# Performance work log

Measured on AMD Instinct MI355X. Metric: run time of the kernel, lower is better.

The kernel has to match this reference:

```python
import jax, jax.numpy as jnp
import numpy as np

# ---- config (matches init_kwargs) ----
SPATIAL_SCALE = 0.0625
POOLED = 7
OUT_DIM = 256
SAMPLE_PER_PART = 4
TRANS_STD = 0.1
PART_SIZE = 7
DEFORM_FC_DIM = 1024
# group_size == 1 -> position-sensitive group index is always 0, channel c == ctop


def _deform_roi_pool(feat, rois, offset, no_trans):
    """Faithful JAX port of DeformablePSROIPoolForward (DCNv2), group_size=1.
    feat: (B,C,H,W), rois: (N,5)=[b,x1,y1,x2,y2], offset: (N,2,P,P) or None.
    Returns (N,C,P,P)."""
    B, C, H, W = feat.shape
    N = rois.shape[0]
    P, S = POOLED, SAMPLE_PER_PART
    dt = feat.dtype
    featT = jnp.transpose(feat, (0, 2, 3, 1))  # (B,H,W,C) for spatial gathers

    b = rois[:, 0].astype(jnp.int32)
    rsw = jnp.round(rois[:, 1]) * SPATIAL_SCALE - 0.5
    rsh = jnp.round(rois[:, 2]) * SPATIAL_SCALE - 0.5
    rew = (jnp.round(rois[:, 3]) + 1.0) * SPATIAL_SCALE - 0.5
    reh = (jnp.round(rois[:, 4]) + 1.0) * SPATIAL_SCALE - 0.5
    roi_w = jnp.maximum(rew - rsw, 0.1)
    roi_h = jnp.maximum(reh - rsh, 0.1)
    bin_h = roi_h / P            # (N,)
    bin_w = roi_w / P
    sub_h = bin_h / S
    sub_w = bin_w / S

    ph = jnp.arange(P)
    pw = jnp.arange(P)
    part_h = jnp.floor(ph.astype(dt) / P * PART_SIZE).astype(jnp.int32)  # == ph when part_size==P
    part_w = jnp.floor(pw.astype(dt) / P * PART_SIZE).astype(jnp.int32)

    if no_trans:
        tx = jnp.zeros((N, P, P), dt)
        ty = jnp.zeros((N, P, P), dt)
    else:
        tx = offset[:, 0][:, part_h][:, :, part_w] * TRANS_STD  # (N,P,P)
        ty = offset[:, 1][:, part_h][:, :, part_w] * TRANS_STD

    hstart = ph.astype(dt)[None, :, None] * bin_h[:, None, None] + rsh[:, None, None] + ty * roi_h[:, None, None]
    wstart = pw.astype(dt)[None, None, :] * bin_w[:, None, None] + rsw[:, None, None] + tx * roi_w[:, None, None]

    ih = jnp.arange(S).astype(dt)
    iw = jnp.arange(S).astype(dt)
    # sample coords, shape (N,P,P,S,S); ih along axis -2, iw along axis -1
    h = hstart[..., None, None] + ih[:, None] * sub_h[:, None, None, None, None]
    w = wstart[..., None, None] + iw[None, :] * sub_w[:, None, None, None, None]

    valid = (w >= -0.5) & (w <= W - 0.5) & (h >= -0.5) & (h <= H - 0.5)
    hc = jnp.clip(h, 0.0, H - 1.0)
    wc = jnp.clip(w, 0.0, W - 1.0)
    h0 = jnp.floor(hc).astype(jnp.int32)
    w0 = jnp.floor(wc).astype(jnp.int32)
    h1 = jnp.minimum(h0 + 1, H - 1)
    w1 = jnp.minimum(w0 + 1, W - 1)
    lh = hc - h0.astype(dt)
    lw = wc - w0.astype(dt)

    bidx = b[:, None, None, None, None]

    def g(yy, xx):  # (N,P,P,S,S,C)
        return featT[bidx, yy, xx]

    val = (g(h0, w0) * ((1 - lh) * (1 - lw))[..., None]
           + g(h0, w1) * ((1 - lh) * lw)[..., None]
           + g(h1, w0) * (lh * (1 - lw))[..., None]
           + g(h1, w1) * (lh * lw)[..., None])
    val = jnp.where(valid[..., None], val, jnp.zeros((), dt))
    ssum = val.sum(axis=(3, 4))                       # (N,P,P,C)
    cnt = valid.sum(axis=(3, 4)).astype(dt)           # (N,P,P)
    out = jnp.where(cnt[..., None] > 0, ssum / jnp.maximum(cnt, 1.0)[..., None], jnp.zeros((), dt))
    return jnp.transpose(out, (0, 3, 1, 2))           # (N,C,P,P)


def setup_inputs() -> dict:
    key = jax.random.key(0)
    ks = jax.random.split(key, 12)
    B, C, H, W = 2, OUT_DIM, 100, 100
    N = 512
    img = H / SPATIAL_SCALE  # 1600

    feat = jax.random.normal(ks[0], (B, C, H, W), jnp.float32)

    bi = jax.random.randint(ks[1], (N,), 0, B).astype(jnp.float32)
    x1 = jax.random.uniform(ks[2], (N,), jnp.float32, 0.0, img - 420.0)
    y1 = jax.random.uniform(ks[3], (N,), jnp.float32, 0.0, img - 420.0)
    x2 = x1 + jax.random.uniform(ks[4], (N,), jnp.float32, 32.0, 400.0)
    y2 = y1 + jax.random.uniform(ks[5], (N,), jnp.float32, 32.0, 400.0)
    rois = jnp.stack([bi, x1, y1, x2, y2], axis=1)

    fin = POOLED * POOLED * OUT_DIM  # 12544
    w1 = jax.random.normal(ks[6], (DEFORM_FC_DIM, fin), jnp.float32) / np.sqrt(fin)
    b1 = jnp.zeros((DEFORM_FC_DIM,), jnp.float32)
    w2 = jax.random.normal(ks[7], (DEFORM_FC_DIM, DEFORM_FC_DIM), jnp.float32) / np.sqrt(DEFORM_FC_DIM)
    b2 = jnp.zeros((DEFORM_FC_DIM,), jnp.float32)
    # original init zeroes the last layer; use small random so offsets/mask are non-trivial
    w3 = jax.random.normal(ks[8], (POOLED * POOLED * 3, DEFORM_FC_DIM), jnp.float32) * 0.01
    b3 = jnp.zeros((POOLED * POOLED * 3,), jnp.float32)
    return {"input": feat, "rois": rois, "w1": w1, "b1": b1, "w2": w2, "b2": b2, "w3": w3, "b3": b3}


def reference(input, rois, w1, b1, w2, b2, w3, b3):
    N = rois.shape[0]
    P = POOLED
    # pass 1: plain (no_trans) deformable RoI pooling to predict offsets/mask
    roi0 = _deform_roi_pool(input, rois, None, no_trans=True)      # (N,C,P,P)
    x = roi0.reshape(N, -1)
    x = jax.nn.relu(x @ w1.T + b1)
    x = jax.nn.relu(x @ w2.T + b2)
    om = (x @ w3.T + b3).reshape(N, 3, P, P)
    offset = om[:, 0:2]                                            # (N,2,P,P) [trans_x, trans_y]
    mask = jax.nn.sigmoid(om[:, 2:3])                              # (N,1,P,P)
    # pass 2: deformable pooling with learned offsets, modulated by mask
    out = _deform_roi_pool(input, rois, offset, no_trans=False) * mask
    return out
```

## Files before the change

kernel.cpp:

```cpp
#include <hip/hip_runtime.h>

#define BB 2
#define CC 256
#define HH 100
#define WW 100
#define NROI 512
#define KDIM 12544
#define FC 1024

typedef _Float16 half_t;
typedef _Float16 f16x2 __attribute__((ext_vector_type(2)));
typedef _Float16 f16x8 __attribute__((ext_vector_type(8)));
typedef _Float16 f16x4 __attribute__((ext_vector_type(4)));
typedef float f32x4 __attribute__((ext_vector_type(4)));

__device__ __forceinline__ void gload16(const half_t* g, half_t* l) {
  __builtin_amdgcn_global_load_lds(
      (const __attribute__((address_space(1))) unsigned int*)g,
      (__attribute__((address_space(3))) unsigned int*)l, 16, 0, 0);
}

__global__ __launch_bounds__(256) void prep(const float* __restrict__ feat,
                                            half_t* __restrict__ featT,
                                            const float* __restrict__ w1,
                                            half_t* __restrict__ w1h,
                                            const float* __restrict__ w2,
                                            half_t* __restrict__ w2h) {
  int bid = blockIdx.x;
  if (bid < 12544) {
    int i4 = (bid * 256 + threadIdx.x) * 4;
    float4 v = *(const float4*)(w1 + i4);
    f16x4 o;
    o[0] = (half_t)v.x; o[1] = (half_t)v.y; o[2] = (half_t)v.z; o[3] = (half_t)v.w;
    *(f16x4*)(w1h + i4) = o;
    return;
  }
  bid -= 12544;
  if (bid < 1024) {
    int i4 = (bid * 256 + threadIdx.x) * 4;
    float4 v = *(const float4*)(w2 + i4);
    f16x4 o;
    o[0] = (half_t)v.x; o[1] = (half_t)v.y; o[2] = (half_t)v.z; o[3] = (half_t)v.w;
    *(f16x4*)(w2h + i4) = o;
    return;
  }
  bid -= 1024;
  __shared__ float tile[32][33];
  const int bx = bid % 313;
  const int rem = bid / 313;
  const int by = rem & 7;
  const int bz = rem >> 3;
  const int tx = threadIdx.x & 31, ty = threadIdx.x >> 5;
  const int hw0 = bx * 32;
  const int c0 = by * 32;
  const float* fb = feat + (size_t)bz * CC * (HH * WW);
#pragma unroll
  for (int i = 0; i < 4; i++) {
    int c = c0 + ty + i * 8;
    int hw = hw0 + tx;
    tile[ty + i * 8][tx] = (hw < HH * WW) ? fb[(size_t)c * (HH * WW) + hw] : 0.0f;
  }
  __syncthreads();
  half_t* ob = featT + (size_t)bz * (HH * WW) * CC;
#pragma unroll
  for (int i = 0; i < 4; i++) {
    int hw = hw0 + ty + i * 8;
    int c = c0 + tx;
    if (hw < HH * WW) ob[(size_t)hw * CC + c] = (half_t)tile[tx][ty + i * 8];
  }
}

struct PixW { int idx; float w; };

template <bool PASS2>
__global__ __launch_bounds__(512) void pool_kernel(const half_t* __restrict__ featT,
                                                   const float* __restrict__ rois,
                                                   const float* __restrict__ part3,
                                                   const float* __restrict__ b3,
                                                   half_t* __restrict__ xout,
                                                   float* __restrict__ out) {
  __shared__ __align__(16) PixW s_pix[49 * 32];
  __shared__ int s_cnt[49];
  __shared__ float s_scale[49];
  __shared__ float  s_outf[PASS2 ? KDIM : 1];
  __shared__ half_t s_outh[PASS2 ? 1 : KDIM];

  const int n = blockIdx.x;
  const int tid = threadIdx.x;
  const float* r = rois + n * 5;
  const int b = (int)r[0];
  const float rsw = rintf(r[1]) * 0.0625f - 0.5f;
  const float rsh = rintf(r[2]) * 0.0625f - 0.5f;
  const float rew = (rintf(r[3]) + 1.0f) * 0.0625f - 0.5f;
  const float reh = (rintf(r[4]) + 1.0f) * 0.0625f - 0.5f;
  const float roi_w = fmaxf(rew - rsw, 0.1f);
  const float roi_h = fmaxf(reh - rsh, 0.1f);
  const float bin_h = roi_h / 7.0f, bin_w = roi_w / 7.0f;
  const float sub_h = bin_h * 0.25f, sub_w = bin_w * 0.25f;
  const half_t* fb = featT + (size_t)b * (HH * WW) * CC;

  if (tid < 49) {
    const int p = tid, ph = p / 7, pw = p - ph * 7;
    float tx = 0.0f, ty = 0.0f, mask = 1.0f;
    if (PASS2) {
      float o0 = b3[p], o1 = b3[49 + p], o2 = b3[98 + p];
#pragma unroll
      for (int zz = 0; zz < 8; zz++) {
        const float* pz = part3 + ((size_t)zz * NROI + n) * 147;
        o0 += pz[p]; o1 += pz[49 + p]; o2 += pz[98 + p];
      }
      tx = o0 * 0.1f;
      ty = o1 * 0.1f;
      mask = 1.0f / (1.0f + expf(-o2));
    }
    const float hst = (float)ph * bin_h + rsh + ty * roi_h;
    const float wst = (float)pw * bin_w + rsw + tx * roi_w;
    float wh[6] = {0, 0, 0, 0, 0, 0};
    float hc0 = fminf(fmaxf(hst, 0.0f), 99.0f);
    const int r0 = (int)hc0;
    int rtop = r0;
    float vsh = 0.0f;
#pragma unroll
    for (int i = 0; i < 4; i++) {
      float h = hst + (float)i * sub_h;
      bool v = (h >= -0.5f) && (h <= (float)HH - 0.5f);
      float hc = fminf(fmaxf(h, 0.0f), 99.0f);
      int h0 = (int)hc;
      float lh = hc - (float)h0;
      int h1 = min(h0 + 1, HH - 1);
      if (v) { wh[h0 - r0] += 1.0f - lh; wh[h1 - r0] += lh; vsh += 1.0f; }
      rtop = h1;
    }
    float wwc[6] = {0, 0, 0, 0, 0, 0};
    float wc0 = fminf(fmaxf(wst, 0.0f), 99.0f);
    const int c0 = (int)wc0;
    int ctop = c0;
    float vsw = 0.0f;
#pragma unroll
    for (int j = 0; j < 4; j++) {
      float w = wst + (float)j * sub_w;
      bool v = (w >= -0.5f) && (w <= (float)WW - 0.5f);
      float wc = fminf(fmaxf(w, 0.0f), 99.0f);
      int w0 = (int)wc;
      float lw = wc - (float)w0;
      int w1 = min(w0 + 1, WW - 1);
      if (v) { wwc[w0 - c0] += 1.0f - lw; wwc[w1 - c0] += lw; vsw += 1.0f; }
      ctop = w1;
    }
    const int nr = rtop - r0 + 1, nc = ctop - c0 + 1;
    float cntf = vsh * vsw;
    s_scale[p] = (cntf > 0.0f) ? mask / cntf : 0.0f;
    PixW* dst = &s_pix[p * 32];
    int m = 0;
    for (int ri = 0; ri < nr; ri++) {
      int rowoff = (r0 + ri) * WW + c0;
      for (int ci = 0; ci < nc; ci++) {
        dst[m].idx = (rowoff + ci) * CC;
        dst[m].w = wh[ri] * wwc[ci];
        m++;
      }
    }
    while (m & 7) { dst[m].idx = 0; dst[m].w = 0.0f; m++; }
    s_cnt[p] = m;
  }
  __syncthreads();

  const int wv = tid >> 6;
  const int lane = tid & 63;
  const int half = lane >> 5;
  const int c8 = (lane & 31) * 8;
  for (int p = wv; p < 49; p += 8) {
    const int cnt = s_cnt[p];
    const PixW* cp = &s_pix[p * 32];
    float a0 = 0, a1 = 0, a2 = 0, a3 = 0, a4 = 0, a5 = 0, a6 = 0, a7 = 0;
    for (int q = 0; q < cnt; q += 8) {
      PixW e0 = cp[q + 0 + half];
      PixW e1 = cp[q + 2 + half];
      PixW e2 = cp[q + 4 + half];
      PixW e3 = cp[q + 6 + half];
      f16x8 v0 = *(const f16x8*)(fb + e0.idx + c8);
      f16x8 v1 = *(const f16x8*)(fb + e1.idx + c8);
      f16x8 v2 = *(const f16x8*)(fb + e2.idx + c8);
      f16x8 v3 = *(const f16x8*)(fb + e3.idx + c8);
      a0 += e0.w * (float)v0[0] + e1.w * (float)v1[0] + e2.w * (float)v2[0] + e3.w * (float)v3[0];
      a1 += e0.w * (float)v0[1] + e1.w * (float)v1[1] + e2.w * (float)v2[1] + e3.w * (float)v3[1];
      a2 += e0.w * (float)v0[2] + e1.w * (float)v1[2] + e2.w * (float)v2[2] + e3.w * (float)v3[2];
      a3 += e0.w * (float)v0[3] + e1.w * (float)v1[3] + e2.w * (float)v2[3] + e3.w * (float)v3[3];
      a4 += e0.w * (float)v0[4] + e1.w * (float)v1[4] + e2.w * (float)v2[4] + e3.w * (float)v3[4];
      a5 += e0.w * (float)v0[5] + e1.w * (float)v1[5] + e2.w * (float)v2[5] + e3.w * (float)v3[5];
      a6 += e0.w * (float)v0[6] + e1.w * (float)v1[6] + e2.w * (float)v2[6] + e3.w * (float)v3[6];
      a7 += e0.w * (float)v0[7] + e1.w * (float)v1[7] + e2.w * (float)v2[7] + e3.w * (float)v3[7];
    }
    a0 += __shfl_xor(a0, 32); a1 += __shfl_xor(a1, 32);
    a2 += __shfl_xor(a2, 32); a3 += __shfl_xor(a3, 32);
    a4 += __shfl_xor(a4, 32); a5 += __shfl_xor(a5, 32);
    a6 += __shfl_xor(a6, 32); a7 += __shfl_xor(a7, 32);
    if (half == 0) {
      float sc = s_scale[p];
      a0 *= sc; a1 *= sc; a2 *= sc; a3 *= sc; a4 *= sc; a5 *= sc; a6 *= sc; a7 *= sc;
      if (PASS2) {
        s_outf[(c8 + 0) * 49 + p] = a0;
        s_outf[(c8 + 1) * 49 + p] = a1;
        s_outf[(c8 + 2) * 49 + p] = a2;
        s_outf[(c8 + 3) * 49 + p] = a3;
        s_outf[(c8 + 4) * 49 + p] = a4;
        s_outf[(c8 + 5) * 49 + p] = a5;
        s_outf[(c8 + 6) * 49 + p] = a6;
        s_outf[(c8 + 7) * 49 + p] = a7;
      } else {
        s_outh[(c8 + 0) * 49 + p] = (half_t)a0;
        s_outh[(c8 + 1) * 49 + p] = (half_t)a1;
        s_outh[(c8 + 2) * 49 + p] = (half_t)a2;
        s_outh[(c8 + 3) * 49 + p] = (half_t)a3;
        s_outh[(c8 + 4) * 49 + p] = (half_t)a4;
        s_outh[(c8 + 5) * 49 + p] = (half_t)a5;
        s_outh[(c8 + 6) * 49 + p] = (half_t)a6;
        s_outh[(c8 + 7) * 49 + p] = (half_t)a7;
      }
    }
  }
  __syncthreads();

  if (PASS2) {
    float* ob = out + (size_t)n * KDIM;
    for (int l = tid * 4; l < KDIM; l += 2048)
      *(float4*)(ob + l) = *(const float4*)(s_outf + l);
  } else {
    half_t* ob = xout + (size_t)n * KDIM;
    for (int l = tid * 8; l < KDIM; l += 4096)
      *(f16x8*)(ob + l) = *(const f16x8*)(s_outh + l);
  }
}

template <int SK>
__global__ __launch_bounds__(256, 2) void gemm_lds(const half_t* __restrict__ A,
                                                   const half_t* __restrict__ B,
                                                   float* __restrict__ P, int K) {
  __shared__ half_t As[2][128 * 64];
  __shared__ half_t Bs[2][128 * 64];
  const int d = blockIdx.x + gridDim.x * (blockIdx.y + gridDim.y * blockIdx.z);
  const int g = (d & 7) * (SK * 4) + (d >> 3);
  const int z = g >> 5;
  const int tile = g & 31;
  const int m0 = (tile & 3) * 128;
  const int n0 = (tile >> 2) * 128;
  const int Kc = K / SK;
  const int kbeg = z * Kc;
  const int tid = threadIdx.x;
  const int lane = tid & 63;
  const int wave = tid >> 6;
  const int wm = (wave & 1) * 64;
  const int wn = (wave >> 1) * 64;
  const int fr = lane & 15;
  const int kc0 = lane >> 4;
  const int lr = lane >> 3;
  const int lc = (lane & 7) ^ lr;
  const half_t* Ag = A + (size_t)(m0 + wave * 8 + lr) * K + kbeg + lc * 8;
  const half_t* Bg = B + (size_t)(n0 + wave * 8 + lr) * K + kbeg + lc * 8;
  f32x4 acc[4][4] = {};

  auto stage = [&](int buf, int ko) {
#pragma unroll
    for (int s = 0; s < 4; s++)
      gload16(Ag + (size_t)(32 * s) * K + ko, &As[buf][s * 2048 + wave * 512]);
#pragma unroll
    for (int s = 0; s < 4; s++)
      gload16(Bg + (size_t)(32 * s) * K + ko, &Bs[buf][s * 2048 + wave * 512]);
  };

  const int iters = Kc >> 6;
  stage(0, 0);
  if (iters > 1) {
    stage(1, 64);
    asm volatile("s_waitcnt vmcnt(8)" ::: "memory");
  } else {
    asm volatile("s_waitcnt vmcnt(0)" ::: "memory");
  }
  __builtin_amdgcn_s_barrier();

  for (int it = 0; it < iters; it++) {
    const int cur = it & 1;
#pragma unroll
    for (int ks = 0; ks < 2; ks++) {
      const int swz = ((kc0 + ks * 4) ^ (fr & 7)) * 8;
      f16x8 af[4], bf[4];
#pragma unroll
      for (int i = 0; i < 4; i++) af[i] = *(const f16x8*)&As[cur][(wm + i * 16 + fr) * 64 + swz];
#pragma unroll
      for (int j = 0; j < 4; j++) bf[j] = *(const f16x8*)&Bs[cur][(wn + j * 16 + fr) * 64 + swz];
      __builtin_amdgcn_s_setprio(1);
#pragma unroll
      for (int i = 0; i < 4; i++)
#pragma unroll
        for (int j = 0; j < 4; j++)
          acc[i][j] = __builtin_amdgcn_mfma_f32_16x16x32_f16(af[i], bf[j], acc[i][j], 0, 0, 0);
      __builtin_amdgcn_s_setprio(0);
    }
    asm volatile("s_waitcnt lgkmcnt(0)" ::: "memory");
    __builtin_amdgcn_s_barrier();
    const bool issue = (it + 2 < iters);
    if (issue) stage(cur, (it + 2) * 64);
    if (it + 1 < iters) {
      if (issue) asm volatile("s_waitcnt vmcnt(8)" ::: "memory");
      else       asm volatile("s_waitcnt vmcnt(0)" ::: "memory");
      __builtin_amdgcn_s_barrier();
    }
  }
  float* Pz = P + (((size_t)z * 32 + tile) * 4 + wave) * 4096;
#pragma unroll
  for (int i = 0; i < 4; i++)
#pragma unroll
    for (int j = 0; j < 4; j++)
#pragma unroll
      for (int rr = 0; rr < 4; rr++)
        Pz[((i * 4 + j) * 4 + rr) * 64 + lane] = acc[i][j][rr];
}

template <bool OUT16, bool RELU, int SK>
__global__ __launch_bounds__(256) void reduce_blocked(const float* __restrict__ P,
                                                      const float* __restrict__ bias,
                                                      void* __restrict__ out,
                                                      int MN, int N) {
  int i4 = (blockIdx.x * 256 + threadIdx.x) * 4;
  if (i4 >= MN) return;
  float4 s = *(const float4*)(P + i4);
#pragma unroll
  for (int z = 1; z < SK; z++) {
    float4 t = *(const float4*)(P + (size_t)z * MN + i4);
    s.x += t.x; s.y += t.y; s.z += t.z; s.w += t.w;
  }
  const int lane0 = i4 & 63;
  const int q     = (i4 >> 6) & 63;
  const int wave  = (i4 >> 12) & 3;
  const int bx    = (i4 >> 14) & 3;
  const int by    = (i4 >> 16) & 7;
  const int rr = q & 3, j_ = (q >> 2) & 3, i_ = q >> 4;
  const int row = bx * 128 + (wave & 1) * 64 + i_ * 16 + (lane0 >> 4) * 4 + rr;
  const int col = by * 128 + (wave >> 1) * 64 + j_ * 16 + (lane0 & 15);
  float4 bv = *(const float4*)(bias + col);
  s.x += bv.x; s.y += bv.y; s.z += bv.z; s.w += bv.w;
  if (RELU) {
    s.x = fmaxf(s.x, 0.0f); s.y = fmaxf(s.y, 0.0f);
    s.z = fmaxf(s.z, 0.0f); s.w = fmaxf(s.w, 0.0f);
  }
  size_t o = (size_t)row * N + col;
  if (OUT16) {
    f16x4 ov;
    ov[0] = (half_t)s.x; ov[1] = (half_t)s.y; ov[2] = (half_t)s.z; ov[3] = (half_t)s.w;
    *(f16x4*)((half_t*)out + o) = ov;
  } else {
    *(float4*)((float*)out + o) = s;
  }
}

__global__ __launch_bounds__(192) void gemm3_part(const float* __restrict__ h2,
                                                  const float* __restrict__ w3,
                                                  float* __restrict__ part3) {
  __shared__ float hs[8][128];
  const int n0 = blockIdx.x * 8;
  const int z = blockIdx.y;
  const int tid = threadIdx.x;
  for (int idx = tid; idx < 1024; idx += 192) {
    int nn = idx >> 7, kk = idx & 127;
    hs[nn][kk] = h2[(size_t)(n0 + nn) * FC + z * 128 + kk];
  }
  __syncthreads();
  const int j = tid;
  if (j < 147) {
    const float* wr = w3 + (size_t)j * FC + z * 128;
    float acc[8] = {0, 0, 0, 0, 0, 0, 0, 0};
    for (int k = 0; k < 128; k += 4) {
      float4 wv = *(const float4*)(wr + k);
#pragma unroll
      for (int nn = 0; nn < 8; nn++)
        acc[nn] += hs[nn][k] * wv.x + hs[nn][k + 1] * wv.y +
                   hs[nn][k + 2] * wv.z + hs[nn][k + 3] * wv.w;
    }
#pragma unroll
    for (int nn = 0; nn < 8; nn++)
      part3[((size_t)z * NROI + n0 + nn) * 147 + j] = acc[nn];
  }
}

extern "C" void kernel_launch(void* const* d_in, const int* in_sizes, int n_in,
                              void* d_out, int out_size, void* d_ws, size_t ws_size,
                              hipStream_t stream) {
  const float* feat = (const float*)d_in[0];
  const float* rois = (const float*)d_in[1];
  const float* w1 = (const float*)d_in[2];
  const float* b1 = (const float*)d_in[3];
  const float* w2 = (const float*)d_in[4];
  const float* b2 = (const float*)d_in[5];
  const float* w3 = (const float*)d_in[6];
  const float* b3 = (const float*)d_in[7];
  float* out = (float*)d_out;
  char* ws = (char*)d_ws;

  half_t* featT = (half_t*)ws;
  half_t* xh    = (half_t*)(ws + 10240000);
  half_t* w1h   = (half_t*)(ws + 23085056);
  half_t* w2h   = (half_t*)(ws + 48775168);
  half_t* h1    = (half_t*)(ws + 50872320);
  float*  h2    = (float*)(ws + 51920896);
  float*  part  = (float*)(ws + 54319104);

  const int MN = NROI * FC;

  prep<<<dim3(18576), dim3(256), 0, stream>>>(feat, featT, w1, w1h, w2, w2h);
  pool_kernel<false><<<dim3(NROI), dim3(512), 0, stream>>>(featT, rois, nullptr, nullptr, xh, nullptr);

  gemm_lds<14><<<dim3(4, 8, 14), dim3(256), 0, stream>>>(xh, w1h, part, KDIM);
  reduce_blocked<true, true, 14><<<dim3(MN / 1024), dim3(256), 0, stream>>>(part, b1, (void*)h1, MN, FC);

  gemm_lds<8><<<dim3(4, 8, 8), dim3(256), 0, stream>>>(h1, w2h, part, FC);
  reduce_blocked<false, true, 8><<<dim3(MN / 1024), dim3(256), 0, stream>>>(part, b2, (void*)h2, MN, FC);

  gemm3_part<<<dim3(64, 8), dim3(192), 0, stream>>>(h2, w3, part);
  pool_kernel<true><<<dim3(NROI), dim3(512), 0, stream>>>(featT, rois, part, b3, nullptr, out);
}
```

Before: 220.3 us.

## Fuse layer-2 split-K reduction into gemm3 and unroll pooling gather loop deeper

```diff
diff --git a/kernel.cpp b/kernel.cpp
--- a/kernel.cpp
+++ b/kernel.cpp
@@ -160,7 +160,7 @@
         m++;
       }
     }
-    while (m & 7) { dst[m].idx = 0; dst[m].w = 0.0f; m++; }
+    while (m & 15) { dst[m].idx = 0; dst[m].w = 0.0f; m++; }
     s_cnt[p] = m;
   }
   __syncthreads();
@@ -173,23 +173,39 @@
     const int cnt = s_cnt[p];
     const PixW* cp = &s_pix[p * 32];
     float a0 = 0, a1 = 0, a2 = 0, a3 = 0, a4 = 0, a5 = 0, a6 = 0, a7 = 0;
-    for (int q = 0; q < cnt; q += 8) {
+    for (int q = 0; q < cnt; q += 16) {
       PixW e0 = cp[q + 0 + half];
       PixW e1 = cp[q + 2 + half];
       PixW e2 = cp[q + 4 + half];
       PixW e3 = cp[q + 6 + half];
+      PixW e4 = cp[q + 8 + half];
+      PixW e5 = cp[q + 10 + half];
+      PixW e6 = cp[q + 12 + half];
+      PixW e7 = cp[q + 14 + half];
       f16x8 v0 = *(const f16x8*)(fb + e0.idx + c8);
       f16x8 v1 = *(const f16x8*)(fb + e1.idx + c8);
       f16x8 v2 = *(const f16x8*)(fb + e2.idx + c8);
       f16x8 v3 = *(const f16x8*)(fb + e3.idx + c8);
-      a0 += e0.w * (float)v0[0] + e1.w * (float)v1[0] + e2.w * (float)v2[0] + e3.w * (float)v3[0];
-      a1 += e0.w * (float)v0[1] + e1.w * (float)v1[1] + e2.w * (float)v2[1] + e3.w * (float)v3[1];
-      a2 += e0.w * (float)v0[2] + e1.w * (float)v1[2] + e2.w * (float)v2[2] + e3.w * (float)v3[2];
-      a3 += e0.w * (float)v0[3] + e1.w * (float)v1[3] + e2.w * (float)v2[3] + e3.w * (float)v3[3];
-      a4 += e0.w * (float)v0[4] + e1.w * (float)v1[4] + e2.w * (float)v2[4] + e3.w * (float)v3[4];
-      a5 += e0.w * (float)v0[5] + e1.w * (float)v1[5] + e2.w * (float)v2[5] + e3.w * (float)v3[5];
-      a6 += e0.w * (float)v0[6] + e1.w * (float)v1[6] + e2.w * (float)v2[6] + e3.w * (float)v3[6];
-      a7 += e0.w * (float)v0[7] + e1.w * (float)v1[7] + e2.w * (float)v2[7] + e3.w * (float)v3[7];
+      f16x8 v4 = *(const f16x8*)(fb + e4.idx + c8);
+      f16x8 v5 = *(const f16x8*)(fb + e5.idx + c8);
+      f16x8 v6 = *(const f16x8*)(fb + e6.idx + c8);
+      f16x8 v7 = *(const f16x8*)(fb + e7.idx + c8);
+      a0 += e0.w * (float)v0[0] + e1.w * (float)v1[0] + e2.w * (float)v2[0] + e3.w * (float)v3[0]
+          + e4.w * (float)v4[0] + e5.w * (float)v5[0] + e6.w * (float)v6[0] + e7.w * (float)v7[0];
+      a1 += e0.w * (float)v0[1] + e1.w * (float)v1[1] + e2.w * (float)v2[1] + e3.w * (float)v3[1]
+          + e4.w * (float)v4[1] + e5.w * (float)v5[1] + e6.w * (float)v6[1] + e7.w * (float)v7[1];
+      a2 += e0.w * (float)v0[2] + e1.w * (float)v1[2] + e2.w * (float)v2[2] + e3.w * (float)v3[2]
+          + e4.w * (float)v4[2] + e5.w * (float)v5[2] + e6.w * (float)v6[2] + e7.w * (float)v7[2];
+      a3 += e0.w * (float)v0[3] + e1.w * (float)v1[3] + e2.w * (float)v2[3] + e3.w * (float)v3[3]
+          + e4.w * (float)v4[3] + e5.w * (float)v5[3] + e6.w * (float)v6[3] + e7.w * (float)v7[3];
+      a4 += e0.w * (float)v0[4] + e1.w * (float)v1[4] + e2.w * (float)v2[4] + e3.w * (float)v3[4]
+          + e4.w * (float)v4[4] + e5.w * (float)v5[4] + e6.w * (float)v6[4] + e7.w * (float)v7[4];
+      a5 += e0.w * (float)v0[5] + e1.w * (float)v1[5] + e2.w * (float)v2[5] + e3.w * (float)v3[5]
+          + e4.w * (float)v4[5] + e5.w * (float)v5[5] + e6.w * (float)v6[5] + e7.w * (float)v7[5];
+      a6 += e0.w * (float)v0[6] + e1.w * (float)v1[6] + e2.w * (float)v2[6] + e3.w * (float)v3[6]
+          + e4.w * (float)v4[6] + e5.w * (float)v5[6] + e6.w * (float)v6[6] + e7.w * (float)v7[6];
+      a7 += e0.w * (float)v0[7] + e1.w * (float)v1[7] + e2.w * (float)v2[7] + e3.w * (float)v3[7]
+          + e4.w * (float)v4[7] + e5.w * (float)v5[7] + e6.w * (float)v6[7] + e7.w * (float)v7[7];
     }
     a0 += __shfl_xor(a0, 32); a1 += __shfl_xor(a1, 32);
     a2 += __shfl_xor(a2, 32); a3 += __shfl_xor(a3, 32);
@@ -353,21 +369,45 @@
   }
 }
 
-__global__ __launch_bounds__(192) void gemm3_part(const float* __restrict__ h2,
-                                                  const float* __restrict__ w3,
-                                                  float* __restrict__ part3) {
+__global__ __launch_bounds__(256) void gemm3_fused(const float* __restrict__ part2,
+                                                   const float* __restrict__ b2,
+                                                   const float* __restrict__ w3,
+                                                   float* __restrict__ part3) {
   __shared__ float hs[8][128];
   const int n0 = blockIdx.x * 8;
-  const int z = blockIdx.y;
+  const int z3 = blockIdx.y;
   const int tid = threadIdx.x;
-  for (int idx = tid; idx < 1024; idx += 192) {
-    int nn = idx >> 7, kk = idx & 127;
-    hs[nn][kk] = h2[(size_t)(n0 + nn) * FC + z * 128 + kk];
+  const int MN = NROI * FC;
+  {
+    const int idx4 = tid * 4;
+    const int nn = idx4 >> 7;
+    const int kk = idx4 & 127;
+    const int row = n0 + nn;
+    const int col = z3 * 128 + kk;
+    const int bx = (row >> 7) & 3;
+    const int by = (col >> 7) & 7;
+    const int wv = ((row >> 6) & 1) | (((col >> 6) & 1) << 1);
+    const int q  = ((row >> 4) & 3) * 16 + ((col >> 4) & 3) * 4 + (row & 3);
+    const int l0 = ((row >> 2) & 3) * 16 + (col & 15);
+    const int tile = by * 4 + bx;
+    const size_t base = (size_t)((tile * 4 + wv) * 4096 + q * 64 + l0);
+    float4 s = *(const float4*)(part2 + base);
+#pragma unroll
+    for (int z2 = 1; z2 < 8; z2++) {
+      float4 t = *(const float4*)(part2 + (size_t)z2 * MN + base);
+      s.x += t.x; s.y += t.y; s.z += t.z; s.w += t.w;
+    }
+    float4 bv = *(const float4*)(b2 + col);
+    s.x = fmaxf(s.x + bv.x, 0.0f);
+    s.y = fmaxf(s.y + bv.y, 0.0f);
+    s.z = fmaxf(s.z + bv.z, 0.0f);
+    s.w = fmaxf(s.w + bv.w, 0.0f);
+    *(float4*)(&hs[nn][kk]) = s;
   }
   __syncthreads();
   const int j = tid;
   if (j < 147) {
-    const float* wr = w3 + (size_t)j * FC + z * 128;
+    const float* wr = w3 + (size_t)j * FC + z3 * 128;
     float acc[8] = {0, 0, 0, 0, 0, 0, 0, 0};
     for (int k = 0; k < 128; k += 4) {
       float4 wv = *(const float4*)(wr + k);
@@ -378,7 +418,7 @@
     }
 #pragma unroll
     for (int nn = 0; nn < 8; nn++)
-      part3[((size_t)z * NROI + n0 + nn) * 147 + j] = acc[nn];
+      part3[((size_t)z3 * NROI + n0 + nn) * 147 + j] = acc[nn];
   }
 }
 
@@ -401,8 +441,8 @@
   half_t* w1h   = (half_t*)(ws + 23085056);
   half_t* w2h   = (half_t*)(ws + 48775168);
   half_t* h1    = (half_t*)(ws + 50872320);
-  float*  h2    = (float*)(ws + 51920896);
   float*  part  = (float*)(ws + 54319104);
+  float*  part3 = (float*)(ws + 83679232);
 
   const int MN = NROI * FC;
 
@@ -413,8 +453,7 @@
   reduce_blocked<true, true, 14><<<dim3(MN / 1024), dim3(256), 0, stream>>>(part, b1, (void*)h1, MN, FC);
 
   gemm_lds<8><<<dim3(4, 8, 8), dim3(256), 0, stream>>>(h1, w2h, part, FC);
-  reduce_blocked<false, true, 8><<<dim3(MN / 1024), dim3(256), 0, stream>>>(part, b2, (void*)h2, MN, FC);
-
-  gemm3_part<<<dim3(64, 8), dim3(192), 0, stream>>>(h2, w3, part);
-  pool_kernel<true><<<dim3(NROI), dim3(512), 0, stream>>>(featT, rois, part, b3, nullptr, out);
-}
+
+  gemm3_fused<<<dim3(64, 8), dim3(256), 0, stream>>>(part, b2, w3, part3);
+  pool_kernel<true><<<dim3(NROI), dim3(512), 0, stream>>>(featT, rois, part3, b3, nullptr, out);
+}
```

Result: no change. 218.1 us (-1.0%).
